# Performance work log

Measured on AMD Instinct MI355X. Metric: run time of the kernel, lower is better.

The kernel has to match this reference:

```python
import jax, jax.numpy as jnp
import numpy as np

B, T, C = 8, 2048, 1024
HEAD = 64

def setup_inputs() -> dict:
    key = jax.random.key(0)
    k1, k2 = jax.random.split(key)
    x = jax.random.normal(k1, (B, T, C), dtype=jnp.float32)
    # nn.Linear(dim_embedding, head_size, bias=False) weight: [head_size, dim_embedding]
    W_k = jax.random.normal(k2, (HEAD, C), dtype=jnp.float32) * (C ** -0.5)
    return {"x": x, "W_k": W_k}

def reference(x, W_k):
    # Faithful to source: q, k, v are ALL computed with the `key` projection,
    # and the scale is C**-0.5 (embedding dim), as written in the torch code.
    Bx, Tx, Cx = x.shape
    k = jnp.einsum('btc,hc->bth', x, W_k)   # [B,T,HEAD]
    q = k
    v = k
    scale = Cx ** -0.5
    weight = jnp.einsum('bth,bsh->bts', q, k) * scale  # [B,T,T]
    causal = jnp.tril(jnp.ones((Tx, Tx), dtype=bool))
    weight = jnp.where(causal, weight, -jnp.inf)
    weight = jax.nn.softmax(weight, axis=-1)
    # dropout: eval-mode identity (p=0.2 at train time in the source)
    out = jnp.einsum('bts,bsh->bth', weight, v)  # [B,T,HEAD]
    return out
```

## Files before the change

kernel.cpp:

```cpp
#include <hip/hip_runtime.h>
#include <hip/hip_bf16.h>
#include <math.h>

#define SEQ   2048
#define CDIM  1024
#define HD    64
#define NROW  16384
#define CEXP 0.04508422002778112f

typedef float  f32x4  __attribute__((ext_vector_type(4)));
typedef __bf16 bf16x8 __attribute__((ext_vector_type(8)));
typedef int    i32x4  __attribute__((ext_vector_type(4)));

#define AS1 __attribute__((address_space(1)))
#define AS3 __attribute__((address_space(3)))

static __device__ __forceinline__ unsigned pk2(float a, float b) {
    unsigned ua = __builtin_bit_cast(unsigned, a);
    unsigned ub = __builtin_bit_cast(unsigned, b);
    ua += 0x7fffu + ((ua >> 16) & 1u);
    ub += 0x7fffu + ((ub >> 16) & 1u);
    return (ua >> 16) | (ub & 0xffff0000u);
}

static __device__ __forceinline__ bf16x8 cvt8(f32x4 lo, f32x4 hi) {
    i32x4 w = { (int)pk2(lo[0], lo[1]), (int)pk2(lo[2], lo[3]),
                (int)pk2(hi[0], hi[1]), (int)pk2(hi[2], hi[3]) };
    return __builtin_bit_cast(bf16x8, w);
}

__global__ __launch_bounds__(256) void wconv_kernel(const float* __restrict__ W,
                                                    unsigned* __restrict__ Wb) {
    const int i = blockIdx.x * 256 + threadIdx.x;
    float4 v = *(const float4*)(W + (size_t)i * 4);
    uint2 p = make_uint2(pk2(v.x, v.y), pk2(v.z, v.w));
    *(uint2*)(Wb + (size_t)i * 2) = p;
}

template<int S>
struct XProl {
    static __device__ __forceinline__ void run(f32x4 (&XA)[8], f32x4 (&XB)[8],
                                               unsigned long long xa) {
        constexpr int OFF = S * 128;
        asm volatile("global_load_dwordx4 %0, %2, off offset:%3\n\t"
                     "global_load_dwordx4 %1, %2, off offset:%4"
                     : "=&v"(XA[S]), "=&v"(XB[S])
                     : "v"(xa), "n"(OFF), "n"(OFF + 16)
                     : "memory");
        if constexpr (S + 1 < 8) XProl<S + 1>::run(XA, XB, xa);
    }
};

template<int T>
struct XLoop {
    static __device__ __forceinline__ void run(f32x4 (&XA)[8], f32x4 (&XB)[8],
                                               unsigned long long xa,
                                               const char* const (&wp)[4][2],
                                               f32x4 (&acc)[4]) {
        constexpr int WT = (T < 24) ? 14 : 2 * (31 - T);
        asm volatile("s_waitcnt vmcnt(%0)" :: "n"(WT) : "memory");
        __builtin_amdgcn_sched_barrier(0);
        bf16x8 A = cvt8(XA[T & 7], XB[T & 7]);
        #pragma unroll
        for (int nt = 0; nt < 4; ++nt) {
            bf16x8 B = *(const bf16x8*)(wp[nt][T & 1] + (T >> 1) * 128);
            acc[nt] = __builtin_amdgcn_mfma_f32_16x16x32_bf16(A, B, acc[nt], 0, 0, 0);
        }
        if constexpr (T < 24) {
            constexpr int OFF = (T + 8) * 128;
            asm volatile("global_load_dwordx4 %0, %2, off offset:%3\n\t"
                         "global_load_dwordx4 %1, %2, off offset:%4"
                         : "=&v"(XA[T & 7]), "=&v"(XB[T & 7])
                         : "v"(xa), "n"(OFF), "n"(OFF + 16)
                         : "memory");
        }
        if constexpr (T + 1 < 32) XLoop<T + 1>::run(XA, XB, xa, wp, acc);
    }
};

__global__ __launch_bounds__(256, 1) void proj_kernel(const float* __restrict__ x,
                                                      const unsigned short* __restrict__ Wb,
                                                      unsigned short* __restrict__ Ko,
                                                      uint2* __restrict__ KV2) {
    __shared__ __align__(16) char wlds[131072];

    const int tid = threadIdx.x;
    const int wid = tid >> 6, l = tid & 63, lm = l & 15, lg = l >> 4;
    const int bid = blockIdx.x;

    #pragma unroll
    for (int j = 0; j < 32; ++j) {
        int d = j * 4096 + tid * 16;
        int row = d >> 11, inner = d & 2047;
        int sin_ = inner ^ ((row & 7) << 4);
        const unsigned short* src = Wb + (size_t)row * CDIM + (sin_ >> 1);
        __builtin_amdgcn_global_load_lds((const AS1 void*)src,
                                         (AS3 void*)(wlds + j * 4096 + wid * 1024),
                                         16, 0, 0);
    }

    const int row = bid * 64 + wid * 16 + lm;
    unsigned long long xa =
        (unsigned long long)(const void*)(x + (size_t)row * CDIM + lg * 8);
    f32x4 XA[8], XB[8];
    XProl<0>::run(XA, XB, xa);

    asm volatile("s_waitcnt vmcnt(16)" ::: "memory");
    __builtin_amdgcn_sched_barrier(0);
    __builtin_amdgcn_s_barrier();
    __builtin_amdgcn_sched_barrier(0);

    const int hb = (lm >> 2) & 1;
    const int L  = ((lg ^ (lm & 3)) << 4);
    const char* wp[4][2];
    #pragma unroll
    for (int nt = 0; nt < 4; ++nt) {
        const char* base = wlds + (nt * 16 + lm) * 2048;
        wp[nt][0] = base + hb * 64 + L;
        wp[nt][1] = base + (1 - hb) * 64 + L;
    }

    f32x4 acc[4];
    acc[0] = acc[1] = acc[2] = acc[3] = (f32x4){0.f, 0.f, 0.f, 0.f};
    XLoop<0>::run(XA, XB, xa, wp, acc);

    const size_t m0r = (size_t)bid * 64 + wid * 16;
    #pragma unroll
    for (int nt = 0; nt < 4; ++nt)
        #pragma unroll
        for (int r = 0; r < 4; ++r)
            Ko[(m0r + lg * 4 + r) * HD + nt * 16 + lm] =
                (unsigned short)(pk2(acc[nt][r], 0.f) & 0xffffu);
    const size_t g = (size_t)bid * 4 + wid;
    #pragma unroll
    for (int nt = 0; nt < 4; ++nt)
        KV2[(g * 4 + nt) * 64 + l] =
            make_uint2(pk2(acc[nt][0], acc[nt][1]), pk2(acc[nt][2], acc[nt][3]));
}

struct KT { bf16x8 ka0, ka1; uint2 bv[4]; };

static __device__ __forceinline__ KT load_tile(const unsigned short* __restrict__ Kb,
                                               const uint2* __restrict__ KVb,
                                               int kt, int lm, int lg, int l) {
    KT t;
    const unsigned short* ar = Kb + (size_t)(kt * 16 + lm) * HD + lg * 8;
    t.ka0 = *(const bf16x8*)ar;
    t.ka1 = *(const bf16x8*)(ar + 32);
    const uint2* vp = KVb + (size_t)kt * 256 + l;
    #pragma unroll
    for (int nt = 0; nt < 4; ++nt) t.bv[nt] = vp[nt * 64];
    return t;
}

static __device__ __forceinline__ void proc_tile(const KT& t, bf16x8 bq0, bf16x8 bq1,
                                                 bool diag, int lm, int lg,
                                                 float& ls, f32x4 o[4]) {
    f32x4 s4 = (f32x4){0.f, 0.f, 0.f, 0.f};
    s4 = __builtin_amdgcn_mfma_f32_16x16x32_bf16(t.ka0, bq0, s4, 0, 0, 0);
    s4 = __builtin_amdgcn_mfma_f32_16x16x32_bf16(t.ka1, bq1, s4, 0, 0, 0);
    float s0 = s4[0], s1 = s4[1], s2 = s4[2], s3 = s4[3];
    if (diag) {
        const int kb = lg * 4;
        s0 = (kb + 0 > lm) ? -1e30f : s0;
        s1 = (kb + 1 > lm) ? -1e30f : s1;
        s2 = (kb + 2 > lm) ? -1e30f : s2;
        s3 = (kb + 3 > lm) ? -1e30f : s3;
    }
    float p0 = __builtin_amdgcn_exp2f(s0 * CEXP);
    float p1 = __builtin_amdgcn_exp2f(s1 * CEXP);
    float p2 = __builtin_amdgcn_exp2f(s2 * CEXP);
    float p3 = __builtin_amdgcn_exp2f(s3 * CEXP);
    ls += (p0 + p1) + (p2 + p3);
    bf16x8 pa = { (__bf16)p0, (__bf16)p1, (__bf16)p2, (__bf16)p3,
                  (__bf16)0.f, (__bf16)0.f, (__bf16)0.f, (__bf16)0.f };
    #pragma unroll
    for (int nt = 0; nt < 4; ++nt) {
        i32x4 vw = { (int)t.bv[nt].x, (int)t.bv[nt].y, 0, 0 };
        bf16x8 bvx = __builtin_bit_cast(bf16x8, vw);
        o[nt] = __builtin_amdgcn_mfma_f32_16x16x32_bf16(pa, bvx, o[nt], 0, 0, 0);
    }
}

static __device__ __forceinline__ void flash_qtile(const unsigned short* __restrict__ Kb,
                                                   const uint2* __restrict__ KVb,
                                                   int qt, int w, int lm, int lg, int l,
                                                   float& ls, f32x4 o[4]) {
    if (qt < w) return;
    const unsigned short* qr = Kb + (size_t)(qt * 16 + lm) * HD + lg * 8;
    bf16x8 bq0 = *(const bf16x8*)qr;
    bf16x8 bq1 = *(const bf16x8*)(qr + 32);
    const int last = qt - ((qt - w) & 3);
    KT A = load_tile(Kb, KVb, w, lm, lg, l);
    if (last == w) {
        proc_tile(A, bq0, bq1, last == qt, lm, lg, ls, o);
        return;
    }
    KT B = load_tile(Kb, KVb, w + 4, lm, lg, l);
    int kt = w;
    while (kt + 8 <= last) {
        KT C = load_tile(Kb, KVb, kt + 8, lm, lg, l);
        proc_tile(A, bq0, bq1, false, lm, lg, ls, o);
        A = B; B = C; kt += 4;
    }
    if (kt + 4 <= last) {
        proc_tile(A, bq0, bq1, false, lm, lg, ls, o);
        A = B; kt += 4;
    }
    proc_tile(A, bq0, bq1, last == qt, lm, lg, ls, o);
}

__global__ __launch_bounds__(256, 2) void attn_kernel(const unsigned short* __restrict__ K,
                                                      const uint2* __restrict__ KV2,
                                                      float* __restrict__ out) {
    __shared__ float oS[2][4][16][68];
    __shared__ float lS[2][4][16];
    const int tid = threadIdx.x;
    const int wid = tid >> 6, l = tid & 63, lm = l & 15, lg = l >> 4;
    const int b = blockIdx.x >> 6, i = blockIdx.x & 63;
    const unsigned short* Kb  = K   + (size_t)b * SEQ * HD;
    const uint2*          KVb = KV2 + (size_t)b * 128 * 256;

    #pragma unroll
    for (int s = 0; s < 2; ++s) {
        const int qt = s ? (127 - i) : i;
        float ls = 0.f;
        f32x4 o[4];
        o[0] = o[1] = o[2] = o[3] = (f32x4){0.f, 0.f, 0.f, 0.f};
        flash_qtile(Kb, KVb, qt, wid, lm, lg, l, ls, o);
        ls += __shfl_xor(ls, 16);
        ls += __shfl_xor(ls, 32);
        #pragma unroll
        for (int nt = 0; nt < 4; ++nt)
            #pragma unroll
            for (int r = 0; r < 4; ++r)
                oS[s][wid][lg * 4 + r][nt * 16 + lm] = o[nt][r];
        if (lg == 0) lS[s][wid][lm] = ls;
    }
    __syncthreads();

    const int slot = tid >> 7;
    const int row  = (tid >> 3) & 15;
    const int cg   = tid & 7;
    const int qt   = slot ? (127 - i) : i;
    float L = lS[slot][0][row] + lS[slot][1][row] + lS[slot][2][row] + lS[slot][3][row];
    const float inv = 1.f / L;
    f32x4 a0 = (f32x4){0.f, 0.f, 0.f, 0.f}, a1 = a0;
    #pragma unroll
    for (int w = 0; w < 4; ++w) {
        a0 += *(const f32x4*)&oS[slot][w][row][cg * 8];
        a1 += *(const f32x4*)&oS[slot][w][row][cg * 8 + 4];
    }
    float* op = out + ((size_t)b * SEQ + qt * 16 + row) * HD + cg * 8;
    *(f32x4*)op       = a0 * inv;
    *(f32x4*)(op + 4) = a1 * inv;
}

extern "C" void kernel_launch(void* const* d_in, const int* in_sizes, int n_in,
                              void* d_out, int out_size, void* d_ws, size_t ws_size,
                              hipStream_t stream) {
    const float* x  = (const float*)d_in[0];
    const float* Wk = (const float*)d_in[1];
    float* o        = (float*)d_out;
    unsigned short* Kp = (unsigned short*)d_ws;
    unsigned short* Wb = Kp + (size_t)NROW * HD;
    uint2* KV2 = (uint2*)(Wb + (size_t)HD * CDIM);

    wconv_kernel<<<64, 256, 0, stream>>>(Wk, (unsigned*)Wb);
    proj_kernel<<<256, 256, 0, stream>>>(x, Wb, Kp, KV2);
    attn_kernel<<<512, 256, 0, stream>>>(Kp, KV2, o);
}
```

Measured before the change: 47.90 us.

## Pack two key tiles per PV MFMA and stage K stores through LDS

The attention inner loop now handles two key tiles at a time. Their P values fill all eight bf16 slots of the 16x16x32 MFMA operand, where before half the slots were zero, so each pair of tiles needs four PV MFMAs instead of eight. The P conversion now uses the manual pk2 packing instead of per-element casts. The projection kernel writes K through a small LDS buffer so the global stores become coalesced 16-byte stores. These changes add register pressure and a different prefetch structure with a single-tile tail path.

```diff
diff --git a/kernel.cpp b/kernel.cpp
--- a/kernel.cpp
+++ b/kernel.cpp
@@ -83,6 +83,7 @@
                                                       unsigned short* __restrict__ Ko,
                                                       uint2* __restrict__ KV2) {
     __shared__ __align__(16) char wlds[131072];
+    __shared__ __align__(16) unsigned short tb[4][16][64];
 
     const int tid = threadIdx.x;
     const int wid = tid >> 6, l = tid & 63, lm = l & 15, lg = l >> 4;
@@ -124,13 +125,21 @@
     acc[0] = acc[1] = acc[2] = acc[3] = (f32x4){0.f, 0.f, 0.f, 0.f};
     XLoop<0>::run(XA, XB, xa, wp, acc);
 
-    const size_t m0r = (size_t)bid * 64 + wid * 16;
     #pragma unroll
     for (int nt = 0; nt < 4; ++nt)
         #pragma unroll
         for (int r = 0; r < 4; ++r)
-            Ko[(m0r + lg * 4 + r) * HD + nt * 16 + lm] =
+            tb[wid][lg * 4 + r][nt * 16 + lm] =
                 (unsigned short)(pk2(acc[nt][r], 0.f) & 0xffffu);
+    const size_t m0r = (size_t)bid * 64 + wid * 16;
+    {
+        const char* tbase = (const char*)&tb[wid][0][0];
+        i32x4 v0 = *(const i32x4*)(tbase + l * 16);
+        i32x4 v1 = *(const i32x4*)(tbase + 1024 + l * 16);
+        char* kbase = (char*)(Ko + m0r * HD);
+        *(i32x4*)(kbase + l * 16)        = v0;
+        *(i32x4*)(kbase + 1024 + l * 16) = v1;
+    }
     const size_t g = (size_t)bid * 4 + wid;
     #pragma unroll
     for (int nt = 0; nt < 4; ++nt)
@@ -139,6 +148,7 @@
 }
 
 struct KT { bf16x8 ka0, ka1; uint2 bv[4]; };
+struct KT2 { bf16x8 kaA0, kaA1, kaB0, kaB1; i32x4 bv[4]; };
 
 static __device__ __forceinline__ KT load_tile(const unsigned short* __restrict__ Kb,
                                                const uint2* __restrict__ KVb,
@@ -150,6 +160,26 @@
     const uint2* vp = KVb + (size_t)kt * 256 + l;
     #pragma unroll
     for (int nt = 0; nt < 4; ++nt) t.bv[nt] = vp[nt * 64];
+    return t;
+}
+
+static __device__ __forceinline__ KT2 load_pair(const unsigned short* __restrict__ Kb,
+                                                const uint2* __restrict__ KVb,
+                                                int kt, int lm, int lg, int l) {
+    KT2 t;
+    const unsigned short* arA = Kb + (size_t)(kt * 16 + lm) * HD + lg * 8;
+    const unsigned short* arB = arA + 4 * 16 * HD;
+    t.kaA0 = *(const bf16x8*)arA;
+    t.kaA1 = *(const bf16x8*)(arA + 32);
+    t.kaB0 = *(const bf16x8*)arB;
+    t.kaB1 = *(const bf16x8*)(arB + 32);
+    const uint2* vpA = KVb + (size_t)kt * 256 + l;
+    const uint2* vpB = vpA + 4 * 256;
+    #pragma unroll
+    for (int nt = 0; nt < 4; ++nt) {
+        uint2 a = vpA[nt * 64], b = vpB[nt * 64];
+        t.bv[nt] = (i32x4){ (int)a.x, (int)a.y, (int)b.x, (int)b.y };
+    }
     return t;
 }
 
@@ -172,13 +202,48 @@
     float p2 = __builtin_amdgcn_exp2f(s2 * CEXP);
     float p3 = __builtin_amdgcn_exp2f(s3 * CEXP);
     ls += (p0 + p1) + (p2 + p3);
-    bf16x8 pa = { (__bf16)p0, (__bf16)p1, (__bf16)p2, (__bf16)p3,
-                  (__bf16)0.f, (__bf16)0.f, (__bf16)0.f, (__bf16)0.f };
+    i32x4 pw = { (int)pk2(p0, p1), (int)pk2(p2, p3), 0, 0 };
+    bf16x8 pa = __builtin_bit_cast(bf16x8, pw);
     #pragma unroll
     for (int nt = 0; nt < 4; ++nt) {
         i32x4 vw = { (int)t.bv[nt].x, (int)t.bv[nt].y, 0, 0 };
         bf16x8 bvx = __builtin_bit_cast(bf16x8, vw);
         o[nt] = __builtin_amdgcn_mfma_f32_16x16x32_bf16(pa, bvx, o[nt], 0, 0, 0);
+    }
+}
+
+static __device__ __forceinline__ void proc_pair(const KT2& t, bf16x8 bq0, bf16x8 bq1,
+                                                 bool diagB, int lm, int lg,
+                                                 float& ls, f32x4 o[4]) {
+    f32x4 sa = (f32x4){0.f, 0.f, 0.f, 0.f}, sb = sa;
+    sa = __builtin_amdgcn_mfma_f32_16x16x32_bf16(t.kaA0, bq0, sa, 0, 0, 0);
+    sa = __builtin_amdgcn_mfma_f32_16x16x32_bf16(t.kaA1, bq1, sa, 0, 0, 0);
+    sb = __builtin_amdgcn_mfma_f32_16x16x32_bf16(t.kaB0, bq0, sb, 0, 0, 0);
+    sb = __builtin_amdgcn_mfma_f32_16x16x32_bf16(t.kaB1, bq1, sb, 0, 0, 0);
+    float b0 = sb[0], b1 = sb[1], b2 = sb[2], b3 = sb[3];
+    if (diagB) {
+        const int kb = lg * 4;
+        b0 = (kb + 0 > lm) ? -1e30f : b0;
+        b1 = (kb + 1 > lm) ? -1e30f : b1;
+        b2 = (kb + 2 > lm) ? -1e30f : b2;
+        b3 = (kb + 3 > lm) ? -1e30f : b3;
+    }
+    float pa0 = __builtin_amdgcn_exp2f(sa[0] * CEXP);
+    float pa1 = __builtin_amdgcn_exp2f(sa[1] * CEXP);
+    float pa2 = __builtin_amdgcn_exp2f(sa[2] * CEXP);
+    float pa3 = __builtin_amdgcn_exp2f(sa[3] * CEXP);
+    float pb0 = __builtin_amdgcn_exp2f(b0 * CEXP);
+    float pb1 = __builtin_amdgcn_exp2f(b1 * CEXP);
+    float pb2 = __builtin_amdgcn_exp2f(b2 * CEXP);
+    float pb3 = __builtin_amdgcn_exp2f(b3 * CEXP);
+    ls += ((pa0 + pa1) + (pa2 + pa3)) + ((pb0 + pb1) + (pb2 + pb3));
+    i32x4 pw = { (int)pk2(pa0, pa1), (int)pk2(pa2, pa3),
+                 (int)pk2(pb0, pb1), (int)pk2(pb2, pb3) };
+    bf16x8 pa8 = __builtin_bit_cast(bf16x8, pw);
+    #pragma unroll
+    for (int nt = 0; nt < 4; ++nt) {
+        bf16x8 bvx = __builtin_bit_cast(bf16x8, t.bv[nt]);
+        o[nt] = __builtin_amdgcn_mfma_f32_16x16x32_bf16(pa8, bvx, o[nt], 0, 0, 0);
     }
 }
 
@@ -190,24 +255,28 @@
     const unsigned short* qr = Kb + (size_t)(qt * 16 + lm) * HD + lg * 8;
     bf16x8 bq0 = *(const bf16x8*)qr;
     bf16x8 bq1 = *(const bf16x8*)(qr + 32);
-    const int last = qt - ((qt - w) & 3);
-    KT A = load_tile(Kb, KVb, w, lm, lg, l);
-    if (last == w) {
-        proc_tile(A, bq0, bq1, last == qt, lm, lg, ls, o);
+    const int n = ((qt - w) >> 2) + 1;
+    const bool diagL = (w + 4 * (n - 1)) == qt;
+    int kt = w;
+    if (n == 1) {
+        KT S = load_tile(Kb, KVb, kt, lm, lg, l);
+        proc_tile(S, bq0, bq1, diagL, lm, lg, ls, o);
         return;
     }
-    KT B = load_tile(Kb, KVb, w + 4, lm, lg, l);
-    int kt = w;
-    while (kt + 8 <= last) {
-        KT C = load_tile(Kb, KVb, kt + 8, lm, lg, l);
-        proc_tile(A, bq0, bq1, false, lm, lg, ls, o);
-        A = B; B = C; kt += 4;
-    }
-    if (kt + 4 <= last) {
-        proc_tile(A, bq0, bq1, false, lm, lg, ls, o);
-        A = B; kt += 4;
-    }
-    proc_tile(A, bq0, bq1, last == qt, lm, lg, ls, o);
+    KT2 A = load_pair(Kb, KVb, kt, lm, lg, l);
+    int rem = n;
+    while (rem >= 4) {
+        KT2 B = load_pair(Kb, KVb, kt + 8, lm, lg, l);
+        proc_pair(A, bq0, bq1, false, lm, lg, ls, o);
+        A = B; kt += 8; rem -= 2;
+    }
+    if (rem == 3) {
+        KT S = load_tile(Kb, KVb, kt + 8, lm, lg, l);
+        proc_pair(A, bq0, bq1, false, lm, lg, ls, o);
+        proc_tile(S, bq0, bq1, diagL, lm, lg, ls, o);
+    } else {
+        proc_pair(A, bq0, bq1, diagL, lm, lg, ls, o);
+    }
 }
 
 __global__ __launch_bounds__(256, 2) void attn_kernel(const unsigned short* __restrict__ K,
```

Result: no change. 48.06 us (+0.3%).
